# Optimization experiments

Measured on AMD Instinct MI355X. Metric: run time of the kernel, lower is better.

Reference implementation:

```python
import jax, jax.numpy as jnp
import numpy as np

B, D, C = 4096, 2048, 64
L_HP, D_HP, OMEGA, EPSILON = 0.5, 1.0, 100.0, 0.1
LN_EPS = 1e-5
CLASS_COUNTS = [5000,4500,4050,3645,3280,2952,2657,2391,2152,1937,1743,1569,1412,1271,1144,1029,926,834,750,675,608,547,492,443,399,359,323,291,262,236,212,191,172,155,139,125,113,101,91,82,74,66,60,54,48,43,39,35,32,28,26,23,21,19,17,15,14,12,11,10,9,8,7,7]


def setup_inputs() -> dict:
    key = jax.random.key(0)
    k_x, k_y, k_b, k_u1, k_u2 = jax.random.split(key, 5)
    counts = jnp.asarray(CLASS_COUNTS, dtype=jnp.float32)
    # set_class_weights: tilde_C = 1/log(counts*d + eps), min-max normalized, scaled by l
    tilde = 1.0 / jnp.log(counts * D_HP + EPSILON)
    c = (tilde - jnp.min(tilde)) / (jnp.max(tilde) - jnp.min(tilde)) * L_HP
    # set_fs_classes: 1 where count <= omega
    fs_classes = jnp.where(counts <= OMEGA, 1, 0).astype(jnp.int32)
    x = jax.random.normal(k_x, (B, D), dtype=jnp.float32)
    y = jax.random.randint(k_y, (B,), 0, C)
    beta_idx = jax.random.randint(k_b, (B,), 0, B)
    u1 = jax.random.uniform(k_u1, (B,))
    u2 = jax.random.uniform(k_u2, (B,))
    alpha = jnp.where(u1 > 0.5, u2, jnp.ones((B,), jnp.float32))
    return {"x": x, "y": y, "alpha": alpha, "beta_idx": beta_idx, "c": c, "fs_classes": fs_classes}


def reference(x, y, alpha, beta_idx, c, fs_classes):
    n_batch, dim = x.shape
    num_classes = c.shape[0]
    # --- reconstruct ---
    mu = jnp.mean(x, axis=-1, keepdims=True)
    var = jnp.mean((x - mu) ** 2, axis=-1, keepdims=True)
    x_norm = (x - mu) / jnp.sqrt(var + LN_EPS) / jnp.sqrt(jnp.asarray(dim, x.dtype))
    sim = jnp.matmul(x_norm, x_norm.T)  # [B, B]
    # E[i, j] = eye[i, j] + fs_mask[j]  (broadcast over rows), thresholded to {0, 1}
    fs_mask = fs_classes[y].astype(x.dtype)  # [B]
    E = jnp.eye(n_batch, dtype=x.dtype) + fs_mask[None, :]
    E = jnp.where(E >= 1.0, 1.0, 0.0)
    sim = jax.nn.softmax(sim - 100000.0 * E, axis=-1)
    contrib = c[y]  # [B]
    reconstructions = jnp.matmul(sim, x)  # [B, D]
    R = reconstructions * contrib[:, None] + x * (1.0 - contrib)[:, None]
    # --- pairwise_mix: M @ R with M[i,:] = alpha[i]*e_i + (1-alpha[i])*e_{beta_idx[i]} ---
    y_oh = jax.nn.one_hot(y, num_classes, dtype=x.dtype)
    a = alpha[:, None]
    x_mix = a * R + (1.0 - a) * R[beta_idx]
    y_mix = a * y_oh + (1.0 - a) * y_oh[beta_idx]
    return (x_mix, y_mix)
```

## Files before the change

kernel.cpp:

```cpp
#include <hip/hip_runtime.h>
#include <cstdint>
#include <cstddef>

typedef __bf16 bf16;
typedef __bf16 bf16x8 __attribute__((ext_vector_type(8)));
typedef float floatx4 __attribute__((ext_vector_type(4)));
typedef int intx8 __attribute__((ext_vector_type(8)));

#define NB 4096
#define ND 2048
#define NCLS 64
#define TSTRIDE 144
#define OS 136

__device__ __forceinline__ void stage16(const void* g, void* l) {
  __builtin_amdgcn_global_load_lds(
      (__attribute__((address_space(1))) unsigned int*)g,
      (__attribute__((address_space(3))) unsigned int*)l, 16, 0, 0);
}

__device__ __forceinline__ unsigned char fp8x1(float f) {
  return (unsigned char)(__builtin_amdgcn_cvt_pk_fp8_f32(f, f, 0, false) & 0xFF);
}
__device__ __forceinline__ int fp8x4(float f0, float f1, float f2, float f3) {
  int d = __builtin_amdgcn_cvt_pk_fp8_f32(f0, f1, 0, false);
  return __builtin_amdgcn_cvt_pk_fp8_f32(f2, f3, d, true);
}

__device__ __forceinline__ void gemm_core1(
    const unsigned char* __restrict__ Abase, const int aoff[4],
    const unsigned char* __restrict__ Bbase, const int boff[4],
    const int ldo[4], int nk, unsigned char* __restrict__ As,
    unsigned char* __restrict__ Bs, floatx4 acc[4][4], int wm, int wn,
    int lane) {
  auto STAGE = [&](int k0) {
#pragma unroll
    for (int q = 0; q < 4; ++q) {
      stage16(Abase + (size_t)(aoff[q] + k0), As + ldo[q]);
      stage16(Bbase + (size_t)(boff[q] + k0), Bs + ldo[q]);
    }
  };
  STAGE(0);
  for (int k = 0; k < nk; ++k) {
    __syncthreads();
    intx8 af[4], bf[4];
#pragma unroll
    for (int i = 0; i < 4; ++i) {
      const int ga = (wm * 4 + i) * 2048 + lane * 16;
      const int4 lo = *(const int4*)(As + ga);
      const int4 hi = *(const int4*)(As + ga + 1024);
      af[i][0] = lo.x; af[i][1] = lo.y; af[i][2] = lo.z; af[i][3] = lo.w;
      af[i][4] = hi.x; af[i][5] = hi.y; af[i][6] = hi.z; af[i][7] = hi.w;
    }
#pragma unroll
    for (int i = 0; i < 4; ++i) {
      const int gb = (wn * 4 + i) * 2048 + lane * 16;
      const int4 lo = *(const int4*)(Bs + gb);
      const int4 hi = *(const int4*)(Bs + gb + 1024);
      bf[i][0] = lo.x; bf[i][1] = lo.y; bf[i][2] = lo.z; bf[i][3] = lo.w;
      bf[i][4] = hi.x; bf[i][5] = hi.y; bf[i][6] = hi.z; bf[i][7] = hi.w;
    }
    __syncthreads();
    if (k + 1 < nk) STAGE((k + 1) << 7);
#pragma unroll
    for (int mi = 0; mi < 4; ++mi)
#pragma unroll
      for (int ni = 0; ni < 4; ++ni)
        acc[mi][ni] = __builtin_amdgcn_mfma_scale_f32_16x16x128_f8f6f4(
            af[mi], bf[ni], acc[mi][ni], 0, 0, 0, 127, 0, 127);
  }
}

__device__ __forceinline__ void make_offs(int row0, int rstride, int lane,
                                          int w, int offs[4], int ldo[4]) {
#pragma unroll
  for (int q = 0; q < 4; ++q) {
    const int g = 2 * w + (q >> 1);
    const int c = q & 1;
    offs[q] = (row0 + g * 16 + (lane & 15)) * rstride + (lane >> 4) * 32 +
              c * 16;
    ldo[q] = g * 2048 + c * 1024;
  }
}


__global__ __launch_bounds__(1024) void perm_kernel(
    const int* __restrict__ y, const int* __restrict__ fs,
    const float* __restrict__ c, int* __restrict__ perm,
    int* __restrict__ minfo, float* __restrict__ lrow,
    float* __restrict__ contrib) {
  const int t = threadIdx.x;
  const int base = t * 4;
  int fl[4];
  int cnt = 0;
#pragma unroll
  for (int j = 0; j < 4; ++j) {
    const int yi = y[base + j];
    fl[j] = (fs[yi] == 0) ? 1 : 0;
    cnt += fl[j];
    contrib[base + j] = c[yi];
    lrow[base + j] = 0.0f;
  }
  const int lane = t & 63, w = t >> 6;
  int inc = cnt;
#pragma unroll
  for (int o = 1; o < 64; o <<= 1) {
    int v = __shfl_up(inc, o);
    if (lane >= o) inc += v;
  }
  __shared__ int wsum[16];
  __shared__ int Msh;
  if (lane == 63) wsum[w] = inc;
  __syncthreads();
  int wbase = 0;
  for (int i = 0; i < w; ++i) wbase += wsum[i];
  int pos = wbase + inc - cnt;
#pragma unroll
  for (int j = 0; j < 4; ++j)
    if (fl[j]) perm[pos++] = base + j;
  if (t == 1023) Msh = wbase + inc;
  __syncthreads();
  const int M = Msh;
  const int Mp = (M + 127) & ~127;
  if (t < Mp - M) perm[M + t] = 0;
  if (t == 0) {
    minfo[0] = M;
    minfo[1] = Mp;
    minfo[2] = Mp >> 7;
  }
}

__global__ __launch_bounds__(256) void prep_kernel(
    const float* __restrict__ x, unsigned char* __restrict__ XN8,
    unsigned char* __restrict__ XBT8, const int* __restrict__ perm,
    const int* __restrict__ minfo) {
  __shared__ float tile[64][65];
  const int t = threadIdx.x;

  if (blockIdx.x < NB) {
    const int row = blockIdx.x;
    const float4* xr = (const float4*)(x + (size_t)row * ND);
    float4 v0 = xr[t], v1 = xr[t + 256];
    float s = v0.x + v0.y + v0.z + v0.w + v1.x + v1.y + v1.z + v1.w;
    float q = v0.x * v0.x + v0.y * v0.y + v0.z * v0.z + v0.w * v0.w +
              v1.x * v1.x + v1.y * v1.y + v1.z * v1.z + v1.w * v1.w;
#pragma unroll
    for (int o = 32; o > 0; o >>= 1) {
      s += __shfl_down(s, o);
      q += __shfl_down(q, o);
    }
    const int w = t >> 6;
    if ((t & 63) == 0) { tile[0][w] = s; tile[1][w] = q; }
    __syncthreads();
    s = tile[0][0] + tile[0][1] + tile[0][2] + tile[0][3];
    q = tile[1][0] + tile[1][1] + tile[1][2] + tile[1][3];
    const float mu = s * (1.0f / ND);
    const float var = q * (1.0f / ND) - mu * mu;
    const float sc =
        rsqrtf(var + 1e-5f) * 0.02209708691207961f * 32.0f;

    int* orow = (int*)(XN8 + (size_t)row * ND);
    orow[t] = fp8x4((v0.x - mu) * sc, (v0.y - mu) * sc, (v0.z - mu) * sc,
                    (v0.w - mu) * sc);
    orow[256 + t] = fp8x4((v1.x - mu) * sc, (v1.y - mu) * sc, (v1.z - mu) * sc,
                          (v1.w - mu) * sc);
  } else {
    const int b2 = blockIdx.x - NB;
    const int rb = b2 & 63;
    const int cb = b2 >> 6;
    if (rb * 64 >= minfo[1]) return;
    const int tx = t & 63, ty = t >> 6;
#pragma unroll
    for (int rr = ty; rr < 64; rr += 4)
      tile[rr][tx] = x[(size_t)perm[rb * 64 + rr] * ND + cb * 64 + tx];
    __syncthreads();
    const int ro = t >> 2;
    const int co = t & 3;
    int4 v;
    {
      const int j = co * 16;
      v.x = fp8x4(tile[j + 0][ro], tile[j + 1][ro], tile[j + 2][ro], tile[j + 3][ro]);
      v.y = fp8x4(tile[j + 4][ro], tile[j + 5][ro], tile[j + 6][ro], tile[j + 7][ro]);
      v.z = fp8x4(tile[j + 8][ro], tile[j + 9][ro], tile[j + 10][ro], tile[j + 11][ro]);
      v.w = fp8x4(tile[j + 12][ro], tile[j + 13][ro], tile[j + 14][ro], tile[j + 15][ro]);
    }
    *(int4*)(XBT8 + (size_t)(cb * 64 + ro) * NB + rb * 64 + co * 16) = v;
  }
}

__global__ __launch_bounds__(256, 3) void gemm_sim_kernel(
    const unsigned char* __restrict__ XN8, unsigned char* __restrict__ P8,
    float* __restrict__ lrow, const int* __restrict__ perm,
    const int* __restrict__ minfo) {
  __shared__ unsigned char smem[32768];
  unsigned char* As = smem;
  unsigned char* Bs = smem + 16384;

  const int Mp = minfo[1];
  const int id = blockIdx.x;
  const int xcd = id & 7;
  const int s = id >> 3;
  const int bi = xcd * 4 + (s & 3);
  const int bjc = s >> 2;
  const int n0 = bjc * 128;
  if (n0 >= Mp) return;
  const int M = minfo[0];
  const int m0 = bi * 128;

  const int t = threadIdx.x, w = t >> 6, lane = t & 63;
  const int wm = w >> 1, wn = w & 1, lm = lane & 15, quad = lane >> 4;

  int aoff[4], boff[4], ldo[4];
  make_offs(m0, ND, lane, w, aoff, ldo);
#pragma unroll
  for (int q = 0; q < 4; ++q) {
    const int g = 2 * w + (q >> 1);
    boff[q] = perm[n0 + g * 16 + (lane & 15)] * ND + (lane >> 4) * 32 +
              (q & 1) * 16;
  }

  floatx4 acc[4][4];
#pragma unroll
  for (int i = 0; i < 4; ++i)
#pragma unroll
    for (int j = 0; j < 4; ++j) acc[i][j] = 0.0f;

  gemm_core1(XN8, aoff, XN8, boff, ldo, ND >> 7, As, Bs, acc, wm, wn, lane);

  int pcol[4], valid[4];
#pragma unroll
  for (int ni = 0; ni < 4; ++ni) {
    const int gc = n0 + wn * 64 + ni * 16 + lm;
    valid[ni] = (gc < M) ? 1 : 0;
    pcol[ni] = perm[gc];
  }

  float rs[4][4];
#pragma unroll
  for (int mi = 0; mi < 4; ++mi)
#pragma unroll
    for (int r = 0; r < 4; ++r) rs[mi][r] = 0.0f;

#pragma unroll
  for (int ni = 0; ni < 4; ++ni) {
#pragma unroll
    for (int mi = 0; mi < 4; ++mi) {
#pragma unroll
      for (int r = 0; r < 4; ++r) {
        const int grow = m0 + wm * 64 + mi * 16 + quad * 4 + r;
        const float e = (valid[ni] && grow != pcol[ni])
                            ? __expf(acc[mi][ni][r] * 0.0009765625f)
                            : 0.0f;
        acc[mi][ni][r] = e;
        rs[mi][r] += e;
      }
    }
  }
#pragma unroll
  for (int mi = 0; mi < 4; ++mi)
#pragma unroll
    for (int r = 0; r < 4; ++r) {
      float vsum = rs[mi][r];
      vsum += __shfl_xor(vsum, 1);
      vsum += __shfl_xor(vsum, 2);
      vsum += __shfl_xor(vsum, 4);
      vsum += __shfl_xor(vsum, 8);
      if (lm == 0)
        atomicAdd(&lrow[m0 + wm * 64 + mi * 16 + quad * 4 + r], vsum);
    }

  __syncthreads();
#pragma unroll
  for (int ni = 0; ni < 4; ++ni) {
    const int col = wn * 64 + ni * 16 + lm;
#pragma unroll
    for (int mi = 0; mi < 4; ++mi)
#pragma unroll
      for (int r = 0; r < 4; ++r) {
        const int row = wm * 64 + mi * 16 + quad * 4 + r;
        smem[row * TSTRIDE + col] = fp8x1(acc[mi][ni][r]);
      }
  }
  __syncthreads();
#pragma unroll
  for (int it = 0; it < 4; ++it) {
    const int row = it * 32 + (t >> 3), ch = t & 7;
    int4 v = *(const int4*)(smem + row * TSTRIDE + ch * 16);
    *(int4*)(P8 + (size_t)(m0 + row) * NB + n0 + ch * 16) = v;
  }
}

__global__ __launch_bounds__(256, 3) void gemm_recon_kernel(
    const unsigned char* __restrict__ P8, const unsigned char* __restrict__ XBT8,
    const float* __restrict__ x, const float* __restrict__ lrow,
    const float* __restrict__ contrib, const int* __restrict__ minfo,
    bf16* __restrict__ R) {
  __shared__ unsigned char smem[36864];
  unsigned char* As = smem;
  unsigned char* Bs = smem + 16384;

  const int id = blockIdx.x;
  const int xcd = id & 7;
  const int s = id >> 3;
  const int bx = xcd * 2 + (s & 1);
  const int by = s >> 1;
  const int m0 = by * 128, n0 = bx * 128;

  const int t = threadIdx.x, w = t >> 6, lane = t & 63;
  const int wm = w >> 1, wn = w & 1, lm = lane & 15, quad = lane >> 4;

  int aoff[4], boff[4], ldo[4];
  make_offs(m0, NB, lane, w, aoff, ldo);
  {
    int ldo2[4];
    make_offs(n0, NB, lane, w, boff, ldo2);
  }

  floatx4 acc[4][4];
#pragma unroll
  for (int i = 0; i < 4; ++i)
#pragma unroll
    for (int j = 0; j < 4; ++j) acc[i][j] = 0.0f;

  gemm_core1(P8, aoff, XBT8, boff, ldo, minfo[2], As, Bs, acc, wm, wn, lane);

  __syncthreads();
  bf16* osm = (bf16*)smem;
#pragma unroll
  for (int mi = 0; mi < 4; ++mi) {
#pragma unroll
    for (int r = 0; r < 4; ++r) {
      const int lrow_i = wm * 64 + mi * 16 + quad * 4 + r;
      const int grow = m0 + lrow_i;
      const float inv = 1.0f / lrow[grow];
      const float ci = contrib[grow];
#pragma unroll
      for (int ni = 0; ni < 4; ++ni) {
        const int lcol = wn * 64 + ni * 16 + lm;
        const float rec = acc[mi][ni][r] * inv;
        const float xv = x[(size_t)grow * ND + n0 + lcol];
        osm[lrow_i * OS + lcol] = (bf16)(rec * ci + xv * (1.0f - ci));
      }
    }
  }
  __syncthreads();
#pragma unroll
  for (int it = 0; it < 8; ++it) {
    const int row = it * 16 + (t >> 4), ch = t & 15;
    int4 v = *(const int4*)(osm + row * OS + ch * 8);
    *(int4*)(R + (size_t)(m0 + row) * ND + n0 + ch * 8) = v;
  }
}

__global__ __launch_bounds__(256) void mix_kernel(
    const bf16* __restrict__ R, const float* __restrict__ alpha,
    const int* __restrict__ beta_idx, const int* __restrict__ y,
    float* __restrict__ out) {
  const int i = blockIdx.x, t = threadIdx.x;
  const float a = alpha[i];
  const int bi = beta_idx[i];
  const bf16x8* Ri = (const bf16x8*)(R + (size_t)i * ND);
  const bf16x8* Rb = (const bf16x8*)(R + (size_t)bi * ND);
  const float b = 1.0f - a;
  bf16x8 r = Ri[t], g = Rb[t];
  float4 o0, o1;
  o0.x = a * (float)r[0] + b * (float)g[0];
  o0.y = a * (float)r[1] + b * (float)g[1];
  o0.z = a * (float)r[2] + b * (float)g[2];
  o0.w = a * (float)r[3] + b * (float)g[3];
  o1.x = a * (float)r[4] + b * (float)g[4];
  o1.y = a * (float)r[5] + b * (float)g[5];
  o1.z = a * (float)r[6] + b * (float)g[6];
  o1.w = a * (float)r[7] + b * (float)g[7];
  float4* o = (float4*)(out + (size_t)i * ND + t * 8);
  o[0] = o0;
  o[1] = o1;
  if (t < NCLS) {
    const int yi = y[i], yb = y[bi];
    const float v = a * (t == yi ? 1.0f : 0.0f) + b * (t == yb ? 1.0f : 0.0f);
    out[(size_t)NB * ND + (size_t)i * NCLS + t] = v;
  }
}

extern "C" void kernel_launch(void* const* d_in, const int* in_sizes, int n_in,
                              void* d_out, int out_size, void* d_ws,
                              size_t ws_size, hipStream_t stream) {
  const float* x = (const float*)d_in[0];
  const int* y = (const int*)d_in[1];
  const float* alpha = (const float*)d_in[2];
  const int* beta = (const int*)d_in[3];
  const float* c = (const float*)d_in[4];
  const int* fs = (const int*)d_in[5];
  float* out = (float*)d_out;
  char* ws = (char*)d_ws;

  unsigned char* XN8  = (unsigned char*)(ws + 0);
  unsigned char* XBT8 = (unsigned char*)(ws + 8388608);
  unsigned char* P8   = (unsigned char*)(ws + 16777216);
  bf16* R   = (bf16*)(ws + 33554432);
  float* LR = (float*)(ws + 50331648);
  float* CT = (float*)(ws + 50331648 + 16384);
  int* PERM = (int*)(ws + 50331648 + 32768);
  int* MINFO = (int*)(ws + 50331648 + 49152);

  perm_kernel<<<1, 1024, 0, stream>>>(y, fs, c, PERM, MINFO, LR, CT);
  prep_kernel<<<NB + 2048, 256, 0, stream>>>(x, XN8, XBT8, PERM, MINFO);
  gemm_sim_kernel<<<768, 256, 0, stream>>>(XN8, P8, LR, PERM, MINFO);
  gemm_recon_kernel<<<512, 256, 0, stream>>>(P8, XBT8, x, LR, CT, MINFO, R);
  mix_kernel<<<NB, 256, 0, stream>>>(R, alpha, beta, y, out);
}
```

Before: 209.3 us.

## Double-buffer LDS tiles in both FP8 GEMMs to drop a barrier per k-step

Splits shared memory into two ping-pong A/B buffers so the next k-tile's global-to-LDS load is issued before reading the current tile. This removes the second __syncthreads per iteration and lets the load overlap with the MFMAs. LDS per block doubles to 64 KB and the occupancy hint of 3 is dropped, so fewer blocks may be resident per CU. The sim GEMM grid also shrinks from 768 to 640 blocks, which cuts early-exit blocks that skip the padded columns.

Result: no change. 210.4 us (+0.5%).

```diff
diff --git a/kernel.cpp b/kernel.cpp
--- a/kernel.cpp
+++ b/kernel.cpp
@@ -27,41 +27,45 @@
   return __builtin_amdgcn_cvt_pk_fp8_f32(f2, f3, d, true);
 }
 
-__device__ __forceinline__ void gemm_core1(
+__device__ __forceinline__ void gemm_core_fm(
     const unsigned char* __restrict__ Abase, const int aoff[4],
     const unsigned char* __restrict__ Bbase, const int boff[4],
-    const int ldo[4], int nk, unsigned char* __restrict__ As,
-    unsigned char* __restrict__ Bs, floatx4 acc[4][4], int wm, int wn,
+    const int ldo[4], int nk, unsigned char* __restrict__ As0,
+    unsigned char* __restrict__ Bs0, unsigned char* __restrict__ As1,
+    unsigned char* __restrict__ Bs1, floatx4 acc[4][4], int wm, int wn,
     int lane) {
-  auto STAGE = [&](int k0) {
+  auto STAGE = [&](int k0, unsigned char* As, unsigned char* Bs) {
 #pragma unroll
     for (int q = 0; q < 4; ++q) {
       stage16(Abase + (size_t)(aoff[q] + k0), As + ldo[q]);
       stage16(Bbase + (size_t)(boff[q] + k0), Bs + ldo[q]);
     }
   };
-  STAGE(0);
+  STAGE(0, As0, Bs0);
   for (int k = 0; k < nk; ++k) {
     __syncthreads();
+    if (k + 1 < nk)
+      STAGE((k + 1) << 7, (k & 1) ? As0 : As1, (k & 1) ? Bs0 : Bs1);
+    const unsigned char* Ac = (k & 1) ? As1 : As0;
+    const unsigned char* Bc = (k & 1) ? Bs1 : Bs0;
+
     intx8 af[4], bf[4];
 #pragma unroll
     for (int i = 0; i < 4; ++i) {
       const int ga = (wm * 4 + i) * 2048 + lane * 16;
-      const int4 lo = *(const int4*)(As + ga);
-      const int4 hi = *(const int4*)(As + ga + 1024);
+      const int4 lo = *(const int4*)(Ac + ga);
+      const int4 hi = *(const int4*)(Ac + ga + 1024);
       af[i][0] = lo.x; af[i][1] = lo.y; af[i][2] = lo.z; af[i][3] = lo.w;
       af[i][4] = hi.x; af[i][5] = hi.y; af[i][6] = hi.z; af[i][7] = hi.w;
     }
 #pragma unroll
     for (int i = 0; i < 4; ++i) {
       const int gb = (wn * 4 + i) * 2048 + lane * 16;
-      const int4 lo = *(const int4*)(Bs + gb);
-      const int4 hi = *(const int4*)(Bs + gb + 1024);
+      const int4 lo = *(const int4*)(Bc + gb);
+      const int4 hi = *(const int4*)(Bc + gb + 1024);
       bf[i][0] = lo.x; bf[i][1] = lo.y; bf[i][2] = lo.z; bf[i][3] = lo.w;
       bf[i][4] = hi.x; bf[i][5] = hi.y; bf[i][6] = hi.z; bf[i][7] = hi.w;
     }
-    __syncthreads();
-    if (k + 1 < nk) STAGE((k + 1) << 7);
 #pragma unroll
     for (int mi = 0; mi < 4; ++mi)
 #pragma unroll
@@ -188,13 +192,15 @@
   }
 }
 
-__global__ __launch_bounds__(256, 3) void gemm_sim_kernel(
+__global__ __launch_bounds__(256) void gemm_sim_kernel(
     const unsigned char* __restrict__ XN8, unsigned char* __restrict__ P8,
     float* __restrict__ lrow, const int* __restrict__ perm,
     const int* __restrict__ minfo) {
-  __shared__ unsigned char smem[32768];
-  unsigned char* As = smem;
-  unsigned char* Bs = smem + 16384;
+  __shared__ unsigned char smem[65536];
+  unsigned char* As0 = smem;
+  unsigned char* Bs0 = smem + 16384;
+  unsigned char* As1 = smem + 32768;
+  unsigned char* Bs1 = smem + 49152;
 
   const int Mp = minfo[1];
   const int id = blockIdx.x;
@@ -225,7 +231,8 @@
 #pragma unroll
     for (int j = 0; j < 4; ++j) acc[i][j] = 0.0f;
 
-  gemm_core1(XN8, aoff, XN8, boff, ldo, ND >> 7, As, Bs, acc, wm, wn, lane);
+  gemm_core_fm(XN8, aoff, XN8, boff, ldo, ND >> 7, As0, Bs0, As1, Bs1, acc,
+               wm, wn, lane);
 
   int pcol[4], valid[4];
 #pragma unroll
@@ -290,14 +297,16 @@
   }
 }
 
-__global__ __launch_bounds__(256, 3) void gemm_recon_kernel(
+__global__ __launch_bounds__(256) void gemm_recon_kernel(
     const unsigned char* __restrict__ P8, const unsigned char* __restrict__ XBT8,
     const float* __restrict__ x, const float* __restrict__ lrow,
     const float* __restrict__ contrib, const int* __restrict__ minfo,
     bf16* __restrict__ R) {
-  __shared__ unsigned char smem[36864];
-  unsigned char* As = smem;
-  unsigned char* Bs = smem + 16384;
+  __shared__ unsigned char smem[65536];
+  unsigned char* As0 = smem;
+  unsigned char* Bs0 = smem + 16384;
+  unsigned char* As1 = smem + 32768;
+  unsigned char* Bs1 = smem + 49152;
 
   const int id = blockIdx.x;
   const int xcd = id & 7;
@@ -322,7 +331,8 @@
 #pragma unroll
     for (int j = 0; j < 4; ++j) acc[i][j] = 0.0f;
 
-  gemm_core1(P8, aoff, XBT8, boff, ldo, minfo[2], As, Bs, acc, wm, wn, lane);
+  gemm_core_fm(P8, aoff, XBT8, boff, ldo, minfo[2], As0, Bs0, As1, Bs1, acc,
+               wm, wn, lane);
 
   __syncthreads();
   bf16* osm = (bf16*)smem;
@@ -405,7 +415,7 @@
 
   perm_kernel<<<1, 1024, 0, stream>>>(y, fs, c, PERM, MINFO, LR, CT);
   prep_kernel<<<NB + 2048, 256, 0, stream>>>(x, XN8, XBT8, PERM, MINFO);
-  gemm_sim_kernel<<<768, 256, 0, stream>>>(XN8, P8, LR, PERM, MINFO);
+  gemm_sim_kernel<<<640, 256, 0, stream>>>(XN8, P8, LR, PERM, MINFO);
   gemm_recon_kernel<<<512, 256, 0, stream>>>(P8, XBT8, x, LR, CT, MINFO, R);
   mix_kernel<<<NB, 256, 0, stream>>>(R, alpha, beta, y, out);
 }
```

## Double-buffer B tiles in LDS with XOR swizzle, load A fragments directly from global

Applied to the files above, without the earlier changes.

The shared GEMM core now reads A fragments straight from global memory and stages only B tiles into LDS. B is double-buffered with an XOR-swizzled layout, so one barrier per k-step replaces two and the next tile's load overlaps the MFMAs. The recon kernel's block-to-XCD mapping is changed, the sim grid shrinks from 768 to 640 blocks, and the mix kernel handles two rows per block. Direct global A loads can add latency to the MFMA loop, and the smaller sim grid relies on the valid column range fitting in fewer blocks.

Result: slower. 213.5 us (+2.0%).

```diff
diff --git a/kernel.cpp b/kernel.cpp
--- a/kernel.cpp
+++ b/kernel.cpp
@@ -27,59 +27,55 @@
   return __builtin_amdgcn_cvt_pk_fp8_f32(f2, f3, d, true);
 }
 
-__device__ __forceinline__ void gemm_core1(
-    const unsigned char* __restrict__ Abase, const int aoff[4],
-    const unsigned char* __restrict__ Bbase, const int boff[4],
-    const int ldo[4], int nk, unsigned char* __restrict__ As,
-    unsigned char* __restrict__ Bs, floatx4 acc[4][4], int wm, int wn,
-    int lane) {
-  auto STAGE = [&](int k0) {
-#pragma unroll
-    for (int q = 0; q < 4; ++q) {
-      stage16(Abase + (size_t)(aoff[q] + k0), As + ldo[q]);
-      stage16(Bbase + (size_t)(boff[q] + k0), Bs + ldo[q]);
-    }
+__device__ __forceinline__ void gemm_core128(
+    const unsigned char* __restrict__ Abase, int astride, int arow0,
+    const unsigned char* __restrict__ Bbase, const int boff[4], int nk,
+    unsigned char* __restrict__ Bs0, unsigned char* __restrict__ Bs1,
+    floatx4 acc[4][4], int w, int lane) {
+  const int wm = w >> 1, wn = w & 1;
+  const int lm = lane & 15, quad = lane >> 4;
+
+  int aoffs[4];
+#pragma unroll
+  for (int i = 0; i < 4; ++i)
+    aoffs[i] = (arow0 + wm * 64 + i * 16 + lm) * astride + quad * 32;
+
+  auto STAGEB = [&](int k0, unsigned char* Bs) {
+#pragma unroll
+    for (int q = 0; q < 4; ++q)
+      stage16(Bbase + (size_t)(boff[q] + k0), Bs + w * 4096 + q * 1024);
   };
-  STAGE(0);
+
+  STAGEB(0, Bs0);
   for (int k = 0; k < nk; ++k) {
     __syncthreads();
+    if (k + 1 < nk) STAGEB((k + 1) << 7, (k & 1) ? Bs0 : Bs1);
+    const unsigned char* Bc = (k & 1) ? Bs1 : Bs0;
+
     intx8 af[4], bf[4];
 #pragma unroll
     for (int i = 0; i < 4; ++i) {
-      const int ga = (wm * 4 + i) * 2048 + lane * 16;
-      const int4 lo = *(const int4*)(As + ga);
-      const int4 hi = *(const int4*)(As + ga + 1024);
+      const int4 lo = *(const int4*)(Abase + (size_t)(aoffs[i] + (k << 7)));
+      const int4 hi =
+          *(const int4*)(Abase + (size_t)(aoffs[i] + (k << 7) + 16));
       af[i][0] = lo.x; af[i][1] = lo.y; af[i][2] = lo.z; af[i][3] = lo.w;
       af[i][4] = hi.x; af[i][5] = hi.y; af[i][6] = hi.z; af[i][7] = hi.w;
     }
 #pragma unroll
     for (int i = 0; i < 4; ++i) {
-      const int gb = (wn * 4 + i) * 2048 + lane * 16;
-      const int4 lo = *(const int4*)(Bs + gb);
-      const int4 hi = *(const int4*)(Bs + gb + 1024);
+      const int row = wn * 64 + i * 16 + lm;
+      const int c0 = (quad * 2) ^ (row & 7);
+      const int4 lo = *(const int4*)(Bc + row * 128 + c0 * 16);
+      const int4 hi = *(const int4*)(Bc + row * 128 + (c0 ^ 1) * 16);
       bf[i][0] = lo.x; bf[i][1] = lo.y; bf[i][2] = lo.z; bf[i][3] = lo.w;
       bf[i][4] = hi.x; bf[i][5] = hi.y; bf[i][6] = hi.z; bf[i][7] = hi.w;
     }
-    __syncthreads();
-    if (k + 1 < nk) STAGE((k + 1) << 7);
 #pragma unroll
     for (int mi = 0; mi < 4; ++mi)
 #pragma unroll
       for (int ni = 0; ni < 4; ++ni)
         acc[mi][ni] = __builtin_amdgcn_mfma_scale_f32_16x16x128_f8f6f4(
             af[mi], bf[ni], acc[mi][ni], 0, 0, 0, 127, 0, 127);
-  }
-}
-
-__device__ __forceinline__ void make_offs(int row0, int rstride, int lane,
-                                          int w, int offs[4], int ldo[4]) {
-#pragma unroll
-  for (int q = 0; q < 4; ++q) {
-    const int g = 2 * w + (q >> 1);
-    const int c = q & 1;
-    offs[q] = (row0 + g * 16 + (lane & 15)) * rstride + (lane >> 4) * 32 +
-              c * 16;
-    ldo[q] = g * 2048 + c * 1024;
   }
 }
 
@@ -193,8 +189,8 @@
     float* __restrict__ lrow, const int* __restrict__ perm,
     const int* __restrict__ minfo) {
   __shared__ unsigned char smem[32768];
-  unsigned char* As = smem;
-  unsigned char* Bs = smem + 16384;
+  unsigned char* Bs0 = smem;
+  unsigned char* Bs1 = smem + 16384;
 
   const int Mp = minfo[1];
   const int id = blockIdx.x;
@@ -210,13 +206,13 @@
   const int t = threadIdx.x, w = t >> 6, lane = t & 63;
   const int wm = w >> 1, wn = w & 1, lm = lane & 15, quad = lane >> 4;
 
-  int aoff[4], boff[4], ldo[4];
-  make_offs(m0, ND, lane, w, aoff, ldo);
+  int boff[4];
 #pragma unroll
   for (int q = 0; q < 4; ++q) {
-    const int g = 2 * w + (q >> 1);
-    boff[q] = perm[n0 + g * 16 + (lane & 15)] * ND + (lane >> 4) * 32 +
-              (q & 1) * 16;
+    const int slot = w * 256 + q * 64 + lane;
+    const int row = slot >> 3;
+    const int cc = (slot & 7) ^ (row & 7);
+    boff[q] = perm[n0 + row] * ND + cc * 16;
   }
 
   floatx4 acc[4][4];
@@ -225,7 +221,7 @@
 #pragma unroll
     for (int j = 0; j < 4; ++j) acc[i][j] = 0.0f;
 
-  gemm_core1(XN8, aoff, XN8, boff, ldo, ND >> 7, As, Bs, acc, wm, wn, lane);
+  gemm_core128(XN8, ND, m0, XN8, boff, ND >> 7, Bs0, Bs1, acc, w, lane);
 
   int pcol[4], valid[4];
 #pragma unroll
@@ -296,24 +292,26 @@
     const float* __restrict__ contrib, const int* __restrict__ minfo,
     bf16* __restrict__ R) {
   __shared__ unsigned char smem[36864];
-  unsigned char* As = smem;
-  unsigned char* Bs = smem + 16384;
+  unsigned char* Bs0 = smem;
+  unsigned char* Bs1 = smem + 16384;
 
   const int id = blockIdx.x;
   const int xcd = id & 7;
   const int s = id >> 3;
-  const int bx = xcd * 2 + (s & 1);
-  const int by = s >> 1;
+  const int by = xcd * 4 + (s & 3);
+  const int bx = s >> 2;
   const int m0 = by * 128, n0 = bx * 128;
 
   const int t = threadIdx.x, w = t >> 6, lane = t & 63;
   const int wm = w >> 1, wn = w & 1, lm = lane & 15, quad = lane >> 4;
 
-  int aoff[4], boff[4], ldo[4];
-  make_offs(m0, NB, lane, w, aoff, ldo);
-  {
-    int ldo2[4];
-    make_offs(n0, NB, lane, w, boff, ldo2);
+  int boff[4];
+#pragma unroll
+  for (int q = 0; q < 4; ++q) {
+    const int slot = w * 256 + q * 64 + lane;
+    const int row = slot >> 3;
+    const int cc = (slot & 7) ^ (row & 7);
+    boff[q] = (n0 + row) * NB + cc * 16;
   }
 
   floatx4 acc[4][4];
@@ -322,7 +320,7 @@
 #pragma unroll
     for (int j = 0; j < 4; ++j) acc[i][j] = 0.0f;
 
-  gemm_core1(P8, aoff, XBT8, boff, ldo, minfo[2], As, Bs, acc, wm, wn, lane);
+  gemm_core128(P8, NB, m0, XBT8, boff, minfo[2], Bs0, Bs1, acc, w, lane);
 
   __syncthreads();
   bf16* osm = (bf16*)smem;
@@ -356,29 +354,33 @@
     const bf16* __restrict__ R, const float* __restrict__ alpha,
     const int* __restrict__ beta_idx, const int* __restrict__ y,
     float* __restrict__ out) {
-  const int i = blockIdx.x, t = threadIdx.x;
-  const float a = alpha[i];
-  const int bi = beta_idx[i];
-  const bf16x8* Ri = (const bf16x8*)(R + (size_t)i * ND);
-  const bf16x8* Rb = (const bf16x8*)(R + (size_t)bi * ND);
-  const float b = 1.0f - a;
-  bf16x8 r = Ri[t], g = Rb[t];
-  float4 o0, o1;
-  o0.x = a * (float)r[0] + b * (float)g[0];
-  o0.y = a * (float)r[1] + b * (float)g[1];
-  o0.z = a * (float)r[2] + b * (float)g[2];
-  o0.w = a * (float)r[3] + b * (float)g[3];
-  o1.x = a * (float)r[4] + b * (float)g[4];
-  o1.y = a * (float)r[5] + b * (float)g[5];
-  o1.z = a * (float)r[6] + b * (float)g[6];
-  o1.w = a * (float)r[7] + b * (float)g[7];
-  float4* o = (float4*)(out + (size_t)i * ND + t * 8);
-  o[0] = o0;
-  o[1] = o1;
-  if (t < NCLS) {
-    const int yi = y[i], yb = y[bi];
-    const float v = a * (t == yi ? 1.0f : 0.0f) + b * (t == yb ? 1.0f : 0.0f);
-    out[(size_t)NB * ND + (size_t)i * NCLS + t] = v;
+  const int t = threadIdx.x;
+#pragma unroll
+  for (int rr = 0; rr < 2; ++rr) {
+    const int i = blockIdx.x * 2 + rr;
+    const float a = alpha[i];
+    const int bi = beta_idx[i];
+    const bf16x8* Ri = (const bf16x8*)(R + (size_t)i * ND);
+    const bf16x8* Rb = (const bf16x8*)(R + (size_t)bi * ND);
+    const float b = 1.0f - a;
+    bf16x8 r = Ri[t], g = Rb[t];
+    float4 o0, o1;
+    o0.x = a * (float)r[0] + b * (float)g[0];
+    o0.y = a * (float)r[1] + b * (float)g[1];
+    o0.z = a * (float)r[2] + b * (float)g[2];
+    o0.w = a * (float)r[3] + b * (float)g[3];
+    o1.x = a * (float)r[4] + b * (float)g[4];
+    o1.y = a * (float)r[5] + b * (float)g[5];
+    o1.z = a * (float)r[6] + b * (float)g[6];
+    o1.w = a * (float)r[7] + b * (float)g[7];
+    float4* o = (float4*)(out + (size_t)i * ND + t * 8);
+    o[0] = o0;
+    o[1] = o1;
+    if (t < NCLS) {
+      const int yi = y[i], yb = y[bi];
+      const float v = a * (t == yi ? 1.0f : 0.0f) + b * (t == yb ? 1.0f : 0.0f);
+      out[(size_t)NB * ND + (size_t)i * NCLS + t] = v;
+    }
   }
 }
 
@@ -405,7 +407,7 @@
 
   perm_kernel<<<1, 1024, 0, stream>>>(y, fs, c, PERM, MINFO, LR, CT);
   prep_kernel<<<NB + 2048, 256, 0, stream>>>(x, XN8, XBT8, PERM, MINFO);
-  gemm_sim_kernel<<<768, 256, 0, stream>>>(XN8, P8, LR, PERM, MINFO);
+  gemm_sim_kernel<<<640, 256, 0, stream>>>(XN8, P8, LR, PERM, MINFO);
   gemm_recon_kernel<<<512, 256, 0, stream>>>(P8, XBT8, x, LR, CT, MINFO, R);
-  mix_kernel<<<NB, 256, 0, stream>>>(R, alpha, beta, y, out);
-}
+  mix_kernel<<<NB / 2, 256, 0, stream>>>(R, alpha, beta, y, out);
+}
```
